# Optimization experiments

Measured on AMD Instinct MI355X. Metric: run time of the kernel, lower is better.

Reference implementation:

```python
import jax, jax.numpy as jnp
import numpy as np

EPS = 1e-10

def _xavier(key, shape, gain=1.414):
    fan_in, fan_out = shape[0], shape[1]
    bound = gain * np.sqrt(6.0 / (fan_in + fan_out))
    return jax.random.uniform(key, shape, jnp.float32, -bound, bound)

def setup_inputs() -> dict:
    key = jax.random.key(0)
    ks = jax.random.split(key, 6)
    N, nfeat, nhid, nclass = 8192, 500, 64, 10
    x = jax.random.normal(ks[0], (N, nfeat), jnp.float32)
    adj = jax.random.uniform(ks[1], (N, N), jnp.float32)
    W1 = _xavier(ks[2], (nfeat, nhid))
    a1 = _xavier(ks[3], (2 * nhid, 1))
    W2 = _xavier(ks[4], (nhid, nclass))
    a2 = _xavier(ks[5], (2 * nclass, 1))
    return {"x": x, "adj": adj, "W1": W1, "a1": a1, "W2": W2, "a2": a2}

def _gat_layer(x, adj, W, a):
    # h: [N, F]
    h = x @ W
    F_out = W.shape[1]
    # e[i,j] = sigmoid(a[:F].h_i + a[F:].h_j)  (equivalent to repeat/cat/matmul)
    s_src = h @ a[:F_out, 0]   # [N]
    s_dst = h @ a[F_out:, 0]   # [N]
    e = jax.nn.sigmoid(s_src[:, None] + s_dst[None, :])  # [N, N]
    attention = e * adj
    # N != 2708/2709 -> l2 row norm branch
    norm = jnp.sqrt(jnp.sum(attention * attention, axis=1, keepdims=True)) + EPS
    attention = attention / norm
    return attention @ h

def reference(x, adj, W1, a1, W2, a2):
    h1 = _gat_layer(x, adj, W1, a1)
    # dropout is identity in eval mode
    h2 = _gat_layer(h1, adj, W2, a2)
    return jax.nn.log_softmax(h2, axis=1)
```

## Files before the change

kernel.cpp:

```cpp
#include <hip/hip_runtime.h>
#include <hip/hip_bf16.h>
#include <math.h>

typedef __attribute__((ext_vector_type(4))) float f32x4;
typedef __attribute__((ext_vector_type(4))) int   i32x4;
typedef __attribute__((ext_vector_type(8))) short short8;

#define NN 8192
#define LOG2E 1.44269504088896f

__device__ __forceinline__ unsigned f2bfu(float x) {
    unsigned u = __float_as_uint(x);
    u += 0x7FFFu + ((u >> 16) & 1u);
    return u >> 16;
}
__device__ __forceinline__ float expneg(float s) {
    return __builtin_amdgcn_exp2f(-LOG2E * s);
}

#define P1_CHUNK 100
__global__ __launch_bounds__(256) void p1_kernel(
    const float* __restrict__ x, const float* __restrict__ W1,
    const float* __restrict__ a1, float* __restrict__ h,
    float* __restrict__ fsrc, float* __restrict__ edst)
{
    __shared__ float wtile[P1_CHUNK * 64];
    const int lane = threadIdx.x & 63;
    const int w    = threadIdx.x >> 6;
    const int r0   = blockIdx.x * 16 + w * 4;

    float acc[4];
#pragma unroll
    for (int r = 0; r < 4; ++r) acc[r] = 0.f;

    for (int c = 0; c < 5; ++c) {
        const int kb = c * P1_CHUNK;
        __syncthreads();
        for (int idx = threadIdx.x; idx < P1_CHUNK * 64; idx += 256)
            wtile[idx] = W1[kb * 64 + idx];
        __syncthreads();
        for (int kk = 0; kk < P1_CHUNK; kk += 4) {
            float w0 = wtile[(kk + 0) * 64 + lane];
            float w1 = wtile[(kk + 1) * 64 + lane];
            float w2 = wtile[(kk + 2) * 64 + lane];
            float w3 = wtile[(kk + 3) * 64 + lane];
#pragma unroll
            for (int r = 0; r < 4; ++r) {
                f32x4 xv = *(const f32x4*)(x + (size_t)(r0 + r) * 500 + kb + kk);
                acc[r] = fmaf(xv[0], w0, acc[r]);
                acc[r] = fmaf(xv[1], w1, acc[r]);
                acc[r] = fmaf(xv[2], w2, acc[r]);
                acc[r] = fmaf(xv[3], w3, acc[r]);
            }
        }
    }
    float a_s = a1[lane], a_d = a1[64 + lane];
#pragma unroll
    for (int r = 0; r < 4; ++r) {
        h[(size_t)(r0 + r) * 64 + lane] = acc[r];
        float ps = acc[r] * a_s, pd = acc[r] * a_d;
        for (int off = 32; off > 0; off >>= 1) {
            ps += __shfl_down(ps, off); pd += __shfl_down(pd, off);
        }
        if (lane == 0) {
            fsrc[r0 + r] = expneg(ps);
            edst[r0 + r] = expneg(pd);
        }
    }
}

__global__ __launch_bounds__(256) void swizzle_kernel(
    const float* __restrict__ h, short* __restrict__ hB,
    int nblk, int ncols, int total)
{
    int tid = blockIdx.x * 256 + threadIdx.x;
    if (tid >= total) return;
    int i  = tid & 7;
    int l  = (tid >> 3) & 63;
    int t2 = tid >> 9;
    int nb = t2 % nblk;
    int kb = t2 / nblk;
    int row = kb * 32 + (l >> 4) * 8 + i;
    int col = nb * 16 + (l & 15);
    float v = h[(size_t)row * ncols + col];
    hB[tid] = (short)f2bfu(v);
}

template <int NBLK>
__global__ __launch_bounds__(512) void fused_kernel(
    const float* __restrict__ adj, const float* __restrict__ fsrc,
    const float* __restrict__ edst, const short* __restrict__ Bfrag,
    float* __restrict__ outp, float* __restrict__ normpart)
{
    __shared__ __align__(16) short Bs[16 * NBLK * 64 * 8];
    const int tid  = threadIdx.x;
    const int lane = tid & 63;
    const int w    = tid >> 6;
    const int seg  = blockIdx.y;
    const int mb   = blockIdx.x * 8 + w;

    {
        const short8* src = (const short8*)(Bfrag) + (size_t)seg * (16 * NBLK * 64);
        short8* dst = (short8*)Bs;
#pragma unroll
        for (int j = 0; j < 2 * NBLK; ++j)
            dst[tid + 512 * j] = src[tid + 512 * j];
    }
    __syncthreads();

    const int r = lane >> 2;
    const int q = lane & 3;

    const float F_i = fsrc[mb * 16 + r];
    const float* arow = adj + (size_t)(mb * 16 + r) * NN;

    const int fg = lane >> 4;
    const int fr = lane & 15;
    const int s0 = fr * 4 + (fg & 1) * 2;
    const int s1 = s0 + 1;
    const bool lowhalf = (fg < 2);

    f32x4 acc[NBLK];
#pragma unroll
    for (int nb = 0; nb < NBLK; ++nb) acc[nb] = (f32x4){0.f, 0.f, 0.f, 0.f};
    float nacc = 0.f;

    for (int k = 0; k < 16; ++k) {
        const int col0 = (seg * 16 + k) * 32;
        f32x4 a0 = *(const f32x4*)(arow + col0 + q * 4);
        f32x4 a1 = *(const f32x4*)(arow + col0 + 16 + q * 4);
        f32x4 e0 = *(const f32x4*)(edst + col0 + q * 4);
        f32x4 e1 = *(const f32x4*)(edst + col0 + 16 + q * 4);

        float v[8];
#pragma unroll
        for (int t = 0; t < 4; ++t) {
            float sg  = __builtin_amdgcn_rcpf(fmaf(F_i, e0[t], 1.0f));
            float att = sg * a0[t];
            nacc = fmaf(att, att, nacc);
            v[t] = att;
        }
#pragma unroll
        for (int t = 0; t < 4; ++t) {
            float sg  = __builtin_amdgcn_rcpf(fmaf(F_i, e1[t], 1.0f));
            float att = sg * a1[t];
            nacc = fmaf(att, att, nacc);
            v[4 + t] = att;
        }
        int d0 = (int)(f2bfu(v[0]) | (f2bfu(v[1]) << 16));
        int d1 = (int)(f2bfu(v[2]) | (f2bfu(v[3]) << 16));
        int d2 = (int)(f2bfu(v[4]) | (f2bfu(v[5]) << 16));
        int d3 = (int)(f2bfu(v[6]) | (f2bfu(v[7]) << 16));

        int p00 = __shfl(d0, s0, 64), p01 = __shfl(d1, s0, 64);
        int p10 = __shfl(d0, s1, 64), p11 = __shfl(d1, s1, 64);
        int q00 = __shfl(d2, s0, 64), q01 = __shfl(d3, s0, 64);
        int q10 = __shfl(d2, s1, 64), q11 = __shfl(d3, s1, 64);
        i32x4 wv;
        wv[0] = lowhalf ? p00 : q00;
        wv[1] = lowhalf ? p01 : q01;
        wv[2] = lowhalf ? p10 : q10;
        wv[3] = lowhalf ? p11 : q11;
        short8 af = *(short8*)&wv;

#pragma unroll
        for (int nb = 0; nb < NBLK; ++nb) {
            short8 bf = *(const short8*)&Bs[((k * NBLK + nb) * 64 + lane) * 8];
            acc[nb] = __builtin_amdgcn_mfma_f32_16x16x32_bf16(af, bf, acc[nb], 0, 0, 0);
        }
    }

    nacc += __shfl_xor(nacc, 1);
    nacc += __shfl_xor(nacc, 2);
    if (q == 0) normpart[(mb * 16 + r) * 16 + seg] = nacc;

    constexpr int F = NBLK * 16;
#pragma unroll
    for (int nb = 0; nb < NBLK; ++nb)
#pragma unroll
        for (int rr = 0; rr < 4; ++rr)
            outp[((size_t)seg * NN + mb * 16 + fg * 4 + rr) * F + nb * 16 + fr]
                = acc[nb][rr];
}

__global__ __launch_bounds__(256) void r1_kernel(
    const float* __restrict__ outp, const float* __restrict__ normpart,
    float* __restrict__ h1)
{
    int tid = blockIdx.x * 256 + threadIdx.x;
    int i = tid >> 6, f = tid & 63;
    float s = 0.f;
#pragma unroll
    for (int sg = 0; sg < 16; ++sg)
        s += outp[((size_t)sg * NN + i) * 64 + f];
    float n = 0.f;
#pragma unroll
    for (int p = 0; p < 16; ++p) n += normpart[i * 16 + p];
    h1[tid] = s / (sqrtf(n) + 1e-10f);
}

__global__ __launch_bounds__(256) void p2_kernel(
    const float* __restrict__ h1, const float* __restrict__ W2,
    const float* __restrict__ a2, float* __restrict__ z,
    float* __restrict__ fsrc2, float* __restrict__ edst2)
{
    int i = blockIdx.x * 256 + threadIdx.x;
    if (i >= NN) return;
    float zz[10];
#pragma unroll
    for (int c = 0; c < 10; ++c) zz[c] = 0.f;
    for (int f = 0; f < 64; ++f) {
        float hv = h1[(size_t)i * 64 + f];
#pragma unroll
        for (int c = 0; c < 10; ++c) zz[c] = fmaf(hv, W2[f * 10 + c], zz[c]);
    }
    float s1 = 0.f, s2 = 0.f;
#pragma unroll
    for (int c = 0; c < 10; ++c) {
        s1 = fmaf(zz[c], a2[c], s1);
        s2 = fmaf(zz[c], a2[10 + c], s2);
        z[(size_t)i * 16 + c] = zz[c];
    }
#pragma unroll
    for (int c = 10; c < 16; ++c) z[(size_t)i * 16 + c] = 0.f;
    fsrc2[i] = expneg(s1);
    edst2[i] = expneg(s2);
}

__global__ __launch_bounds__(256) void r2_kernel(
    const float* __restrict__ outp, const float* __restrict__ normpart,
    float* __restrict__ out)
{
    int i = blockIdx.x * 256 + threadIdx.x;
    if (i >= NN) return;
    float n = 0.f;
#pragma unroll
    for (int p = 0; p < 16; ++p) n += normpart[i * 16 + p];
    float inv = 1.0f / (sqrtf(n) + 1e-10f);
    float v[10];
    float m = -1e30f;
#pragma unroll
    for (int c = 0; c < 10; ++c) {
        float s = 0.f;
#pragma unroll
        for (int sg = 0; sg < 16; ++sg)
            s += outp[((size_t)sg * NN + i) * 16 + c];
        v[c] = s * inv;
        m = fmaxf(m, v[c]);
    }
    float es = 0.f;
#pragma unroll
    for (int c = 0; c < 10; ++c) es += expf(v[c] - m);
    float lse = m + logf(es);
#pragma unroll
    for (int c = 0; c < 10; ++c) out[(size_t)i * 10 + c] = v[c] - lse;
}

extern "C" void kernel_launch(void* const* d_in, const int* in_sizes, int n_in,
                              void* d_out, int out_size, void* d_ws, size_t ws_size,
                              hipStream_t stream)
{
    const float* x   = (const float*)d_in[0];
    const float* adj = (const float*)d_in[1];
    const float* W1  = (const float*)d_in[2];
    const float* a1  = (const float*)d_in[3];
    const float* W2  = (const float*)d_in[4];
    const float* a2  = (const float*)d_in[5];
    float* out = (float*)d_out;

    char* ws = (char*)d_ws;
    size_t off = 0;
    auto alloc = [&](size_t bytes) -> void* {
        void* p = ws + off;
        off += (bytes + 255) & ~(size_t)255;
        return p;
    };
    float* h      = (float*)alloc((size_t)NN * 64 * 4);
    float* fsrc1  = (float*)alloc((size_t)NN * 4);
    float* edst1  = (float*)alloc((size_t)NN * 4);
    short* hB1    = (short*)alloc((size_t)NN * 64 * 2);
    float* outp1  = (float*)alloc((size_t)16 * NN * 64 * 4);
    float* normp1 = (float*)alloc((size_t)NN * 16 * 4);
    float* h1     = (float*)alloc((size_t)NN * 64 * 4);
    float* z      = (float*)alloc((size_t)NN * 16 * 4);
    float* fsrc2  = (float*)alloc((size_t)NN * 4);
    float* edst2  = (float*)alloc((size_t)NN * 4);
    short* zB     = (short*)alloc((size_t)NN * 16 * 2);
    float* outp2  = (float*)alloc((size_t)16 * NN * 16 * 4);
    float* normp2 = (float*)alloc((size_t)NN * 16 * 4);

    hipLaunchKernelGGL(p1_kernel, dim3(NN / 16), dim3(256), 0, stream,
                       x, W1, a1, h, fsrc1, edst1);
    hipLaunchKernelGGL(swizzle_kernel, dim3(2048), dim3(256), 0, stream,
                       h, hB1, 4, 64, NN * 64);
    hipLaunchKernelGGL((fused_kernel<4>), dim3(64, 16), dim3(512), 0, stream,
                       adj, fsrc1, edst1, hB1, outp1, normp1);
    hipLaunchKernelGGL(r1_kernel, dim3(2048), dim3(256), 0, stream,
                       outp1, normp1, h1);
    hipLaunchKernelGGL(p2_kernel, dim3(32), dim3(256), 0, stream,
                       h1, W2, a2, z, fsrc2, edst2);
    hipLaunchKernelGGL(swizzle_kernel, dim3(512), dim3(256), 0, stream,
                       z, zB, 1, 16, NN * 16);
    hipLaunchKernelGGL((fused_kernel<1>), dim3(64, 16), dim3(512), 0, stream,
                       adj, fsrc2, edst2, zB, outp2, normp2);
    hipLaunchKernelGGL(r2_kernel, dim3(32), dim3(256), 0, stream,
                       outp2, normp2, out);
}
```

Baseline: 209.3 us.

## Write bf16 copy of adjacency in layer one and reuse it in layer two

Result: slower. 234.0 us (+11.8%).

```diff
diff --git a/kernel.cpp b/kernel.cpp
--- a/kernel.cpp
+++ b/kernel.cpp
@@ -86,13 +86,14 @@
     hB[tid] = (short)f2bfu(v);
 }
 
-template <int NBLK>
-__global__ __launch_bounds__(512) void fused_kernel(
+__global__ __launch_bounds__(512, 4) void fused1_kernel(
     const float* __restrict__ adj, const float* __restrict__ fsrc,
     const float* __restrict__ edst, const short* __restrict__ Bfrag,
-    float* __restrict__ outp, float* __restrict__ normpart)
-{
-    __shared__ __align__(16) short Bs[16 * NBLK * 64 * 8];
+    short* __restrict__ adjBp, float* __restrict__ outp,
+    float* __restrict__ normpart)
+{
+    __shared__ __align__(16) short Bs[16 * 4 * 64 * 8];
+    __shared__ __align__(16) float Es[512];
     const int tid  = threadIdx.x;
     const int lane = tid & 63;
     const int w    = tid >> 6;
@@ -100,11 +101,12 @@
     const int mb   = blockIdx.x * 8 + w;
 
     {
-        const short8* src = (const short8*)(Bfrag) + (size_t)seg * (16 * NBLK * 64);
+        const short8* src = (const short8*)(Bfrag) + (size_t)seg * (16 * 4 * 64);
         short8* dst = (short8*)Bs;
 #pragma unroll
-        for (int j = 0; j < 2 * NBLK; ++j)
+        for (int j = 0; j < 8; ++j)
             dst[tid + 512 * j] = src[tid + 512 * j];
+        Es[tid] = edst[seg * 512 + tid];
     }
     __syncthreads();
 
@@ -113,6 +115,7 @@
 
     const float F_i = fsrc[mb * 16 + r];
     const float* arow = adj + (size_t)(mb * 16 + r) * NN;
+    short* abrow = adjBp + (size_t)(mb * 16 + r) * NN;
 
     const int fg = lane >> 4;
     const int fr = lane & 15;
@@ -120,17 +123,24 @@
     const int s1 = s0 + 1;
     const bool lowhalf = (fg < 2);
 
-    f32x4 acc[NBLK];
-#pragma unroll
-    for (int nb = 0; nb < NBLK; ++nb) acc[nb] = (f32x4){0.f, 0.f, 0.f, 0.f};
+    f32x4 acc[4];
+#pragma unroll
+    for (int nb = 0; nb < 4; ++nb) acc[nb] = (f32x4){0.f, 0.f, 0.f, 0.f};
     float nacc = 0.f;
 
     for (int k = 0; k < 16; ++k) {
         const int col0 = (seg * 16 + k) * 32;
         f32x4 a0 = *(const f32x4*)(arow + col0 + q * 4);
         f32x4 a1 = *(const f32x4*)(arow + col0 + 16 + q * 4);
-        f32x4 e0 = *(const f32x4*)(edst + col0 + q * 4);
-        f32x4 e1 = *(const f32x4*)(edst + col0 + 16 + q * 4);
+        f32x4 e0 = *(const f32x4*)&Es[k * 32 + q * 4];
+        f32x4 e1 = *(const f32x4*)&Es[k * 32 + 16 + q * 4];
+
+        i32x4 ab;
+        ab[0] = (int)(f2bfu(a0[0]) | (f2bfu(a0[1]) << 16));
+        ab[1] = (int)(f2bfu(a0[2]) | (f2bfu(a0[3]) << 16));
+        ab[2] = (int)(f2bfu(a1[0]) | (f2bfu(a1[1]) << 16));
+        ab[3] = (int)(f2bfu(a1[2]) | (f2bfu(a1[3]) << 16));
+        *(i32x4*)(abrow + col0 + q * 8) = ab;
 
         float v[8];
 #pragma unroll
@@ -164,8 +174,8 @@
         short8 af = *(short8*)&wv;
 
 #pragma unroll
-        for (int nb = 0; nb < NBLK; ++nb) {
-            short8 bf = *(const short8*)&Bs[((k * NBLK + nb) * 64 + lane) * 8];
+        for (int nb = 0; nb < 4; ++nb) {
+            short8 bf = *(const short8*)&Bs[((k * 4 + nb) * 64 + lane) * 8];
             acc[nb] = __builtin_amdgcn_mfma_f32_16x16x32_bf16(af, bf, acc[nb], 0, 0, 0);
         }
     }
@@ -174,13 +184,106 @@
     nacc += __shfl_xor(nacc, 2);
     if (q == 0) normpart[(mb * 16 + r) * 16 + seg] = nacc;
 
-    constexpr int F = NBLK * 16;
-#pragma unroll
-    for (int nb = 0; nb < NBLK; ++nb)
+#pragma unroll
+    for (int nb = 0; nb < 4; ++nb)
 #pragma unroll
         for (int rr = 0; rr < 4; ++rr)
-            outp[((size_t)seg * NN + mb * 16 + fg * 4 + rr) * F + nb * 16 + fr]
+            outp[((size_t)seg * NN + mb * 16 + fg * 4 + rr) * 64 + nb * 16 + fr]
                 = acc[nb][rr];
+}
+
+__global__ __launch_bounds__(512, 4) void fused2_kernel(
+    const short* __restrict__ adjBp, const float* __restrict__ fsrc,
+    const float* __restrict__ edst, const short* __restrict__ Bfrag,
+    float* __restrict__ outp, float* __restrict__ normpart)
+{
+    __shared__ __align__(16) short Bs[16 * 64 * 8];
+    __shared__ __align__(16) float Es[512];
+    const int tid  = threadIdx.x;
+    const int lane = tid & 63;
+    const int w    = tid >> 6;
+    const int seg  = blockIdx.y;
+    const int mb   = blockIdx.x * 8 + w;
+
+    {
+        const short8* src = (const short8*)(Bfrag) + (size_t)seg * (16 * 64);
+        short8* dst = (short8*)Bs;
+#pragma unroll
+        for (int j = 0; j < 2; ++j)
+            dst[tid + 512 * j] = src[tid + 512 * j];
+        Es[tid] = edst[seg * 512 + tid];
+    }
+    __syncthreads();
+
+    const int r = lane >> 2;
+    const int q = lane & 3;
+
+    const float F_i = fsrc[mb * 16 + r];
+    const short* abrow = adjBp + (size_t)(mb * 16 + r) * NN;
+
+    const int fg = lane >> 4;
+    const int fr = lane & 15;
+    const int s0 = fr * 4 + (fg & 1) * 2;
+    const int s1 = s0 + 1;
+    const bool lowhalf = (fg < 2);
+
+    f32x4 acc = (f32x4){0.f, 0.f, 0.f, 0.f};
+    float nacc = 0.f;
+
+    for (int k = 0; k < 16; ++k) {
+        const int col0 = (seg * 16 + k) * 32;
+        i32x4 ab = *(const i32x4*)(abrow + col0 + q * 8);
+        f32x4 e0 = *(const f32x4*)&Es[k * 32 + q * 4];
+        f32x4 e1 = *(const f32x4*)&Es[k * 32 + 16 + q * 4];
+
+        float a[8];
+#pragma unroll
+        for (int t = 0; t < 4; ++t) {
+            a[2 * t]     = __uint_as_float(((unsigned)ab[t]) << 16);
+            a[2 * t + 1] = __uint_as_float(((unsigned)ab[t]) & 0xFFFF0000u);
+        }
+        float v[8];
+#pragma unroll
+        for (int t = 0; t < 4; ++t) {
+            float sg  = __builtin_amdgcn_rcpf(fmaf(F_i, e0[t], 1.0f));
+            float att = sg * a[t];
+            nacc = fmaf(att, att, nacc);
+            v[t] = att;
+        }
+#pragma unroll
+        for (int t = 0; t < 4; ++t) {
+            float sg  = __builtin_amdgcn_rcpf(fmaf(F_i, e1[t], 1.0f));
+            float att = sg * a[4 + t];
+            nacc = fmaf(att, att, nacc);
+            v[4 + t] = att;
+        }
+        int d0 = (int)(f2bfu(v[0]) | (f2bfu(v[1]) << 16));
+        int d1 = (int)(f2bfu(v[2]) | (f2bfu(v[3]) << 16));
+        int d2 = (int)(f2bfu(v[4]) | (f2bfu(v[5]) << 16));
+        int d3 = (int)(f2bfu(v[6]) | (f2bfu(v[7]) << 16));
+
+        int p00 = __shfl(d0, s0, 64), p01 = __shfl(d1, s0, 64);
+        int p10 = __shfl(d0, s1, 64), p11 = __shfl(d1, s1, 64);
+        int q00 = __shfl(d2, s0, 64), q01 = __shfl(d3, s0, 64);
+        int q10 = __shfl(d2, s1, 64), q11 = __shfl(d3, s1, 64);
+        i32x4 wv;
+        wv[0] = lowhalf ? p00 : q00;
+        wv[1] = lowhalf ? p01 : q01;
+        wv[2] = lowhalf ? p10 : q10;
+        wv[3] = lowhalf ? p11 : q11;
+        short8 af = *(short8*)&wv;
+
+        short8 bf = *(const short8*)&Bs[(k * 64 + lane) * 8];
+        acc = __builtin_amdgcn_mfma_f32_16x16x32_bf16(af, bf, acc, 0, 0, 0);
+    }
+
+    nacc += __shfl_xor(nacc, 1);
+    nacc += __shfl_xor(nacc, 2);
+    if (q == 0) normpart[(mb * 16 + r) * 16 + seg] = nacc;
+
+#pragma unroll
+    for (int rr = 0; rr < 4; ++rr)
+        outp[((size_t)seg * NN + mb * 16 + fg * 4 + rr) * 16 + fr] = acc[rr];
 }
 
 __global__ __launch_bounds__(256) void r1_kernel(
@@ -275,6 +378,7 @@
         off += (bytes + 255) & ~(size_t)255;
         return p;
     };
+    short* adjBp  = (short*)alloc((size_t)NN * NN * 2);
     float* h      = (float*)alloc((size_t)NN * 64 * 4);
     float* fsrc1  = (float*)alloc((size_t)NN * 4);
     float* edst1  = (float*)alloc((size_t)NN * 4);
@@ -293,16 +397,16 @@
                        x, W1, a1, h, fsrc1, edst1);
     hipLaunchKernelGGL(swizzle_kernel, dim3(2048), dim3(256), 0, stream,
                        h, hB1, 4, 64, NN * 64);
-    hipLaunchKernelGGL((fused_kernel<4>), dim3(64, 16), dim3(512), 0, stream,
-                       adj, fsrc1, edst1, hB1, outp1, normp1);
+    hipLaunchKernelGGL(fused1_kernel, dim3(64, 16), dim3(512), 0, stream,
+                       adj, fsrc1, edst1, hB1, adjBp, outp1, normp1);
     hipLaunchKernelGGL(r1_kernel, dim3(2048), dim3(256), 0, stream,
                        outp1, normp1, h1);
     hipLaunchKernelGGL(p2_kernel, dim3(32), dim3(256), 0, stream,
                        h1, W2, a2, z, fsrc2, edst2);
     hipLaunchKernelGGL(swizzle_kernel, dim3(512), dim3(256), 0, stream,
                        z, zB, 1, 16, NN * 16);
-    hipLaunchKernelGGL((fused_kernel<1>), dim3(64, 16), dim3(512), 0, stream,
-                       adj, fsrc2, edst2, zB, outp2, normp2);
+    hipLaunchKernelGGL(fused2_kernel, dim3(64, 16), dim3(512), 0, stream,
+                       adjBp, fsrc2, edst2, zB, outp2, normp2);
     hipLaunchKernelGGL(r2_kernel, dim3(32), dim3(256), 0, stream,
                        outp2, normp2, out);
 }
```
